# Optimization experiments

Measured on AMD Instinct MI355X. Metric: run time of the kernel, lower is better.

## Reference

```python
import jax, jax.numpy as jnp
import numpy as np

jax.config.update("jax_enable_x64", True)  # module does int64 wraparound hashing

# Derived from BloomFilter(num_items=10_000_000, false_positive_rate=0.01):
#   pre-round num_bits = ceil(1e7 * ln(100) / ln(2)^2) ~= 95,850,584
#   num_hashes = ceil(pre_round_bits / 1e7 * ln(2)) = 7
#   num_bits rounded up to power of two -> 2**27
NUM_BITS = 2 ** 27
BIT_MASK = NUM_BITS - 1
NUM_HASHES = 7
PRIME = 2654435761


def _hash(values):
    """(N,) int64 -> (N, k) bit positions. Matches torch: (v*PRIME + seed) & bit_mask
    (note Python precedence: & binds looser than +). int64 overflow wraps identically."""
    seeds = jnp.arange(NUM_HASHES, dtype=jnp.int64)
    return (values[:, None] * PRIME + seeds[None, :]) & BIT_MASK


def setup_inputs() -> dict:
    key = jax.random.key(0)
    k1, k2 = jax.random.split(key)
    add_values = jax.random.randint(k1, (4_000_000,), 0, 2**31 - 1, dtype=jnp.int64)
    query_values = jax.random.randint(k2, (8_000_000,), 0, 2**31 - 1, dtype=jnp.int64)
    return {"add_values": add_values, "query_values": query_values}


def reference(add_values, query_values):
    # Bit array of NUM_BITS bools. Semantically identical to the packed int64
    # bitset: word w, offset b in torch <-> flat index (w << 6) | b here, and a
    # bitwise-OR of single-bit masks is exactly an idempotent set-True scatter.
    bits = jnp.zeros((NUM_BITS,), dtype=bool)

    # add(): scatter-set all k hash positions of every inserted value
    add_pos = _hash(add_values)  # (M, k)
    bits = bits.at[add_pos.reshape(-1)].set(True)

    # contains(): gather k bits per query and AND-reduce
    q_pos = _hash(query_values)  # (N, k)
    return jnp.all(bits[q_pos], axis=1)  # (N,) bool
```

## Files before the change

kernel.cpp:

```cpp
#include <hip/hip_runtime.h>
#include <stdint.h>


#define NUM_BITS_LOG2 27
#define NUM_BITS (1u << NUM_BITS_LOG2)
#define BIT_MASK (NUM_BITS - 1u)
#define NUM_WORDS (NUM_BITS >> 6)
#define WORD_MASK (NUM_WORDS - 1u)
#define PRIME 2654435761u
#define H_WORDS (NUM_WORDS >> 2)

#define NBUCKETS 512
#define BKT_SHIFT (NUM_BITS_LOG2 - 9)
#define REGION_WORDS (1u << (BKT_SHIFT - 6))
#define H_WORDS_PER_REGION (REGION_WORDS / 4)
#define CAP 8688u
#define CHUNK 8192u
#define BLOCKS_A 512

typedef int vint4 __attribute__((ext_vector_type(4)));
typedef unsigned long long vull2 __attribute__((ext_vector_type(2)));

#define WS_H_ONLY 20971520ull
#define WS_FULL   38766592ull

__global__ __launch_bounds__(512) void init_gcnt_kernel(uint32_t* __restrict__ gcnt) {
    gcnt[threadIdx.x] = 0u;
}

__global__ __launch_bounds__(256) void scatter_kernel(
    const int* __restrict__ vals, int n,
    uint32_t* __restrict__ lists, uint32_t* __restrict__ gcnt)
{
    __shared__ uint32_t hist[NBUCKETS];
    __shared__ uint32_t sc[NBUCKETS];
    __shared__ uint32_t cur[NBUCKETS];
    __shared__ uint32_t gdelta[NBUCKETS];
    __shared__ uint32_t sortbuf[CHUNK];
    const uint32_t tid = threadIdx.x;
    const uint32_t un = (uint32_t)n;
    const uint32_t nchunks = (un + CHUNK - 1u) / CHUNK;

    for (uint32_t c = blockIdx.x; c < nchunks; c += gridDim.x) {
        const uint32_t base = c * CHUNK;
        const bool full = (base + CHUNK <= un);

        hist[tid] = 0u; hist[tid + 256] = 0u;
        __syncthreads();

        vint4 vv[8];
        if (full) {
            const vint4* src = (const vint4*)(vals + base);
            #pragma unroll
            for (int k = 0; k < 8; ++k) vv[k] = src[(uint32_t)k * 256u + tid];
            #pragma unroll
            for (int k = 0; k < 8; ++k) {
                #pragma unroll
                for (int j = 0; j < 4; ++j) {
                    uint32_t p = ((uint32_t)vv[k][j] * PRIME) & BIT_MASK;
                    uint32_t b1 = p >> BKT_SHIFT;
                    atomicAdd(&hist[b1], 1u);
                    uint32_t b2 = ((p + 6u) & BIT_MASK) >> BKT_SHIFT;
                    if (b2 != b1) {
                        uint32_t s2 = atomicAdd(&gcnt[b2], 1u);
                        if (s2 < CAP) lists[b2 * CAP + s2] = p;
                    }
                }
            }
        } else {
            #pragma unroll
            for (int k = 0; k < 32; ++k) {
                uint32_t idx = base + (uint32_t)k * 256u + tid;
                if (idx < un) {
                    uint32_t p = ((uint32_t)vals[idx] * PRIME) & BIT_MASK;
                    uint32_t b1 = p >> BKT_SHIFT;
                    atomicAdd(&hist[b1], 1u);
                    uint32_t b2 = ((p + 6u) & BIT_MASK) >> BKT_SHIFT;
                    if (b2 != b1) {
                        uint32_t s2 = atomicAdd(&gcnt[b2], 1u);
                        if (s2 < CAP) lists[b2 * CAP + s2] = p;
                    }
                }
            }
        }
        __syncthreads();

        sc[tid] = hist[tid]; sc[tid + 256] = hist[tid + 256];
        __syncthreads();
        for (uint32_t d = 1; d < NBUCKETS; d <<= 1) {
            uint32_t v0 = (tid >= d) ? sc[tid - d] : 0u;
            uint32_t v1 = (tid + 256u >= d) ? sc[tid + 256u - d] : 0u;
            __syncthreads();
            sc[tid] += v0; sc[tid + 256] += v1;
            __syncthreads();
        }

        #pragma unroll
        for (int q = 0; q < 2; ++q) {
            uint32_t i = tid + (uint32_t)q * 256u;
            uint32_t lb = i ? sc[i - 1] : 0u;
            uint32_t cc = hist[i];
            uint32_t go = cc ? atomicAdd(&gcnt[i], cc) : 0u;
            cur[i] = lb;
            gdelta[i] = i * CAP + go - lb;
        }
        __syncthreads();

        if (full) {
            #pragma unroll
            for (int k = 0; k < 8; ++k) {
                #pragma unroll
                for (int j = 0; j < 4; ++j) {
                    uint32_t p = ((uint32_t)vv[k][j] * PRIME) & BIT_MASK;
                    uint32_t b1 = p >> BKT_SHIFT;
                    uint32_t s = atomicAdd(&cur[b1], 1u);
                    sortbuf[s] = p;
                }
            }
        } else {
            #pragma unroll
            for (int k = 0; k < 32; ++k) {
                uint32_t idx = base + (uint32_t)k * 256u + tid;
                if (idx < un) {
                    uint32_t p = ((uint32_t)vals[idx] * PRIME) & BIT_MASK;
                    uint32_t b1 = p >> BKT_SHIFT;
                    uint32_t s = atomicAdd(&cur[b1], 1u);
                    sortbuf[s] = p;
                }
            }
        }
        __syncthreads();

        const uint32_t total = sc[NBUCKETS - 1];
        for (uint32_t i = tid; i < total; i += 256u) {
            uint32_t p = sortbuf[i];
            uint32_t b = p >> BKT_SHIFT;
            uint32_t dst = gdelta[b] + i;
            if (dst - b * CAP < CAP) lists[dst] = p;
        }
        __syncthreads();
    }
}

__device__ __forceinline__ void set_window(unsigned long long* bm, uint32_t p, uint32_t b) {
    int d = (int)((p - (b << BKT_SHIFT)) & BIT_MASK);
    if (d >= (1 << 26)) d -= (1 << 27);
    if (d < -6 || d >= (1 << BKT_SHIFT)) return;
    if (d < 0) {
        atomicOr(&bm[0], 0x7Full >> (uint32_t)(-d));
    } else {
        uint32_t w = (uint32_t)d >> 6, s = (uint32_t)d & 63u;
        atomicOr(&bm[w], 0x7Full << s);
        if (s > 57u) atomicOr(&bm[w + 1], 0x7Full >> (64u - s));
    }
}

__device__ __forceinline__ unsigned long long nib16(unsigned long long a) {
    unsigned long long t = a & (a >> 1);
    unsigned long long u = t & (t >> 2);
    u &= 0x1111111111111111ull;
    u |= u >> 3;  u &= 0x0303030303030303ull;
    u |= u >> 6;  u &= 0x000F000F000F000Full;
    u |= u >> 12; u &= 0x000000FF000000FFull;
    u |= u >> 24; return u & 0xFFFFull;
}

__global__ __launch_bounds__(256) void build_bitmap_kernel(
    const uint32_t* __restrict__ lists, const uint32_t* __restrict__ gcnt,
    unsigned long long* __restrict__ bits, unsigned long long* __restrict__ H)
{
    __shared__ unsigned long long bm[REGION_WORDS + 1];
    const uint32_t b = blockIdx.x, tid = threadIdx.x;
    for (uint32_t i = tid; i < REGION_WORDS + 1; i += 256) bm[i] = 0ull;
    __syncthreads();

    const uint32_t m = min(gcnt[b], CAP);
    const uint32_t base = b * CAP;
    for (uint32_t i = tid; i < m; i += 256) set_window(bm, lists[base + i], b);
    __syncthreads();

    const uint32_t out_base = b * REGION_WORDS;
    for (uint32_t i = tid; i < REGION_WORDS / 2; i += 256) {
        vull2 w; w[0] = bm[i * 2]; w[1] = bm[i * 2 + 1];
        *((vull2*)(bits + out_base) + i) = w;
    }
    const uint32_t h_base = b * H_WORDS_PER_REGION;
    for (uint32_t i = tid; i < H_WORDS_PER_REGION; i += 256) {
        unsigned long long hw = nib16(bm[i * 4])
                              | (nib16(bm[i * 4 + 1]) << 16)
                              | (nib16(bm[i * 4 + 2]) << 32)
                              | (nib16(bm[i * 4 + 3]) << 48);
        H[h_base + i] = hw;
    }
}

__device__ __forceinline__ int query_one_branchy(uint32_t v,
                                                 const unsigned long long* __restrict__ bits) {
    uint32_t p = (v * PRIME) & BIT_MASK;
    uint32_t w = p >> 6, s = p & 63u;
    unsigned long long lo = bits[w];
    unsigned long long win;
    if (s <= 57u) win = lo >> s;
    else win = (lo >> s) | (bits[(w + 1u) & WORD_MASK] << (64u - s));
    return ((win & 0x7Full) == 0x7Full) ? 1 : 0;
}

__global__ __launch_bounds__(256) void query_kernelH(
    const int* __restrict__ vals, int n,
    const unsigned long long* __restrict__ bits,
    const uint32_t* __restrict__ H32, int* __restrict__ out)
{
    int t = blockIdx.x * 256 + threadIdx.x;
    int base = t * 8;
    if (base + 7 < n) {
        vint4 v0 = __builtin_nontemporal_load((const vint4*)(vals + base));
        vint4 v1 = __builtin_nontemporal_load((const vint4*)(vals + base + 4));
        uint32_t p[8], pass[8];
        #pragma unroll
        for (int j = 0; j < 4; ++j) {
            p[j]     = ((uint32_t)v0[j] * PRIME) & BIT_MASK;
            p[j + 4] = ((uint32_t)v1[j] * PRIME) & BIT_MASK;
        }
        #pragma unroll
        for (int j = 0; j < 8; ++j) {
            uint32_t m = ((p[j] + 3u) & BIT_MASK) >> 2;
            pass[j] = (H32[m >> 5] >> (m & 31u)) & 1u;
        }
        unsigned long long lo[8], hi[8];
        uint32_t w[8], s[8];
        #pragma unroll
        for (int j = 0; j < 8; ++j) {
            w[j] = p[j] >> 6; s[j] = p[j] & 63u;
            lo[j] = 0ull; hi[j] = 0ull;
            if (pass[j]) lo[j] = bits[w[j]];
        }
        #pragma unroll
        for (int j = 0; j < 8; ++j) {
            if (pass[j] && s[j] > 57u)
                hi[j] = bits[(w[j] + 1u) & WORD_MASK];
        }
        vint4 r0, r1;
        #pragma unroll
        for (int j = 0; j < 8; ++j) {
            unsigned long long win = (lo[j] >> s[j]) | ((hi[j] << 1) << (63u - s[j]));
            int r = ((win & 0x7Full) == 0x7Full) ? 1 : 0;
            if (j < 4) r0[j] = r; else r1[j - 4] = r;
        }
        __builtin_nontemporal_store(r0, (vint4*)(out + base));
        __builtin_nontemporal_store(r1, (vint4*)(out + base + 4));
    } else {
        for (int j = base; j < n; ++j)
            out[j] = query_one_branchy((uint32_t)vals[j], bits);
    }
}

__global__ __launch_bounds__(256) void zero_bits_kernel(vull2* __restrict__ bits, int n2) {
    int i = blockIdx.x * 256 + threadIdx.x;
    if (i < n2) { vull2 z = {0ull, 0ull}; __builtin_nontemporal_store(z, &bits[i]); }
}

__device__ __forceinline__ void insert_one_atomic(uint32_t v,
                                                  unsigned long long* __restrict__ bits) {
    uint32_t p = (v * PRIME) & BIT_MASK;
    uint32_t w = p >> 6, s = p & 63u;
    atomicOr(bits + w, 0x7Full << s);
    if (s > 57u) atomicOr(bits + ((w + 1u) & WORD_MASK), 0x7Full >> (64u - s));
}

__global__ __launch_bounds__(256) void insert_atomic_kernel(const int* __restrict__ vals, int n,
                                                            unsigned long long* __restrict__ bits) {
    int t = blockIdx.x * 256 + threadIdx.x;
    int base = t * 4;
    if (base + 3 < n) {
        vint4 v = __builtin_nontemporal_load((const vint4*)vals + t);
        insert_one_atomic((uint32_t)v.x, bits);
        insert_one_atomic((uint32_t)v.y, bits);
        insert_one_atomic((uint32_t)v.z, bits);
        insert_one_atomic((uint32_t)v.w, bits);
    } else {
        for (int j = base; j < n; ++j) insert_one_atomic((uint32_t)vals[j], bits);
    }
}

__global__ __launch_bounds__(256) void build_h_kernel(
    const unsigned long long* __restrict__ bits, unsigned long long* __restrict__ H)
{
    uint32_t i = blockIdx.x * 256 + threadIdx.x;
    const vull2* b2 = (const vull2*)bits + (size_t)i * 2;
    vull2 a = b2[0];
    vull2 b = b2[1];
    unsigned long long hw = nib16(a[0])
                          | (nib16(a[1]) << 16)
                          | (nib16(b[0]) << 32)
                          | (nib16(b[1]) << 48);
    H[i] = hw;
}

__global__ __launch_bounds__(256) void query_kernel8(
    const int* __restrict__ vals, int n,
    const unsigned long long* __restrict__ bits, int* __restrict__ out)
{
    int t = blockIdx.x * 256 + threadIdx.x;
    int base = t * 8;
    if (base + 7 < n) {
        vint4 v0 = __builtin_nontemporal_load((const vint4*)(vals + base));
        vint4 v1 = __builtin_nontemporal_load((const vint4*)(vals + base + 4));
        vint4 r0, r1;
        #pragma unroll
        for (int j = 0; j < 8; ++j) {
            uint32_t v = (uint32_t)(j < 4 ? v0[j] : v1[j - 4]);
            int r = query_one_branchy(v, bits);
            if (j < 4) r0[j] = r; else r1[j - 4] = r;
        }
        __builtin_nontemporal_store(r0, (vint4*)(out + base));
        __builtin_nontemporal_store(r1, (vint4*)(out + base + 4));
    } else {
        for (int j = base; j < n; ++j)
            out[j] = query_one_branchy((uint32_t)vals[j], bits);
    }
}

extern "C" void kernel_launch(void* const* d_in, const int* in_sizes, int n_in,
                              void* d_out, int out_size, void* d_ws, size_t ws_size,
                              hipStream_t stream) {
    const int* add_values   = (const int*)d_in[0];
    const int* query_values = (const int*)d_in[1];
    const int n_add   = in_sizes[0];
    const int n_query = in_sizes[1];
    int* out = (int*)d_out;

    uint8_t* ws = (uint8_t*)d_ws;
    unsigned long long* bits = (unsigned long long*)ws;
    unsigned long long* H    = (unsigned long long*)(ws + 16777216);
    uint32_t* lists = (uint32_t*)(ws + 20971520);
    uint32_t* gcnt  = (uint32_t*)(ws + 38764544);

    const int threads = (n_query + 7) / 8;

    if (ws_size >= WS_FULL) {
        init_gcnt_kernel<<<1, 512, 0, stream>>>(gcnt);
        scatter_kernel<<<BLOCKS_A, 256, 0, stream>>>(add_values, n_add, lists, gcnt);
        build_bitmap_kernel<<<NBUCKETS, 256, 0, stream>>>(lists, gcnt, bits, H);
        query_kernelH<<<(threads + 255) / 256, 256, 0, stream>>>(
            query_values, n_query, bits, (const uint32_t*)H, out);
    } else if (ws_size >= WS_H_ONLY) {
        const int n2 = NUM_WORDS / 2;
        zero_bits_kernel<<<(n2 + 255) / 256, 256, 0, stream>>>((vull2*)bits, n2);
        const int threads4 = (n_add + 3) / 4;
        insert_atomic_kernel<<<(threads4 + 255) / 256, 256, 0, stream>>>(
            add_values, n_add, bits);
        build_h_kernel<<<H_WORDS / 256, 256, 0, stream>>>(bits, H);
        query_kernelH<<<(threads + 255) / 256, 256, 0, stream>>>(
            query_values, n_query, bits, (const uint32_t*)H, out);
    } else {
        const int n2 = NUM_WORDS / 2;
        zero_bits_kernel<<<(n2 + 255) / 256, 256, 0, stream>>>((vull2*)bits, n2);
        const int threads4 = (n_add + 3) / 4;
        insert_atomic_kernel<<<(threads4 + 255) / 256, 256, 0, stream>>>(
            add_values, n_add, bits);
        query_kernel8<<<(threads + 255) / 256, 256, 0, stream>>>(
            query_values, n_query, bits, out);
    }
}
```

Measured before the change: 186.4 us.

## Widen scatter/build blocks to 512 threads, use wave-shuffle scan, 16 queries per thread

The scatter kernel now runs 512 threads per block, one block per chunk, and replaces the shared-memory Hillis-Steele scan with a two-level wavefront shuffle scan, cutting barrier count. The bitmap build kernel also runs 512 threads per block. The query kernel handles 16 queries per thread with a pass bitmask and an occupancy hint, giving more memory-level parallelism for the gathers. In exchange it raises register pressure in the query kernel and changes the grid shapes.

After: 196.4 us. +5.4%, slower.

```diff
diff --git a/kernel.cpp b/kernel.cpp
--- a/kernel.cpp
+++ b/kernel.cpp
@@ -16,7 +16,6 @@
 #define H_WORDS_PER_REGION (REGION_WORDS / 4)
 #define CAP 8688u
 #define CHUNK 8192u
-#define BLOCKS_A 512
 
 typedef int vint4 __attribute__((ext_vector_type(4)));
 typedef unsigned long long vull2 __attribute__((ext_vector_type(2)));
@@ -28,16 +27,20 @@
     gcnt[threadIdx.x] = 0u;
 }
 
-__global__ __launch_bounds__(256) void scatter_kernel(
+__global__ __launch_bounds__(512) void scatter_kernel(
     const int* __restrict__ vals, int n,
     uint32_t* __restrict__ lists, uint32_t* __restrict__ gcnt)
 {
     __shared__ uint32_t hist[NBUCKETS];
-    __shared__ uint32_t sc[NBUCKETS];
     __shared__ uint32_t cur[NBUCKETS];
     __shared__ uint32_t gdelta[NBUCKETS];
+    __shared__ uint32_t wsum[8];
+    __shared__ uint32_t wexc[8];
+    __shared__ uint32_t total_s;
     __shared__ uint32_t sortbuf[CHUNK];
     const uint32_t tid = threadIdx.x;
+    const uint32_t lane = tid & 63u;
+    const uint32_t wv = tid >> 6;
     const uint32_t un = (uint32_t)n;
     const uint32_t nchunks = (un + CHUNK - 1u) / CHUNK;
 
@@ -45,16 +48,16 @@
         const uint32_t base = c * CHUNK;
         const bool full = (base + CHUNK <= un);
 
-        hist[tid] = 0u; hist[tid + 256] = 0u;
-        __syncthreads();
-
-        vint4 vv[8];
+        hist[tid] = 0u;
+        __syncthreads();
+
+        vint4 vv[4];
         if (full) {
             const vint4* src = (const vint4*)(vals + base);
             #pragma unroll
-            for (int k = 0; k < 8; ++k) vv[k] = src[(uint32_t)k * 256u + tid];
-            #pragma unroll
-            for (int k = 0; k < 8; ++k) {
+            for (int k = 0; k < 4; ++k) vv[k] = src[(uint32_t)k * 512u + tid];
+            #pragma unroll
+            for (int k = 0; k < 4; ++k) {
                 #pragma unroll
                 for (int j = 0; j < 4; ++j) {
                     uint32_t p = ((uint32_t)vv[k][j] * PRIME) & BIT_MASK;
@@ -69,8 +72,8 @@
             }
         } else {
             #pragma unroll
-            for (int k = 0; k < 32; ++k) {
-                uint32_t idx = base + (uint32_t)k * 256u + tid;
+            for (int k = 0; k < 16; ++k) {
+                uint32_t idx = base + (uint32_t)k * 512u + tid;
                 if (idx < un) {
                     uint32_t p = ((uint32_t)vals[idx] * PRIME) & BIT_MASK;
                     uint32_t b1 = p >> BKT_SHIFT;
@@ -85,30 +88,37 @@
         }
         __syncthreads();
 
-        sc[tid] = hist[tid]; sc[tid + 256] = hist[tid + 256];
-        __syncthreads();
-        for (uint32_t d = 1; d < NBUCKETS; d <<= 1) {
-            uint32_t v0 = (tid >= d) ? sc[tid - d] : 0u;
-            uint32_t v1 = (tid + 256u >= d) ? sc[tid + 256u - d] : 0u;
-            __syncthreads();
-            sc[tid] += v0; sc[tid + 256] += v1;
-            __syncthreads();
-        }
-
-        #pragma unroll
-        for (int q = 0; q < 2; ++q) {
-            uint32_t i = tid + (uint32_t)q * 256u;
-            uint32_t lb = i ? sc[i - 1] : 0u;
-            uint32_t cc = hist[i];
-            uint32_t go = cc ? atomicAdd(&gcnt[i], cc) : 0u;
-            cur[i] = lb;
-            gdelta[i] = i * CAP + go - lb;
-        }
+        const uint32_t c0 = hist[tid];
+        uint32_t x = c0;
+        #pragma unroll
+        for (uint32_t d = 1; d < 64; d <<= 1) {
+            uint32_t y = __shfl_up(x, d, 64);
+            if (lane >= d) x += y;
+        }
+        if (lane == 63u) wsum[wv] = x;
+        __syncthreads();
+        if (wv == 0) {
+            uint32_t t8 = (lane < 8u) ? wsum[lane] : 0u;
+            #pragma unroll
+            for (uint32_t d = 1; d < 8; d <<= 1) {
+                uint32_t y = __shfl_up(t8, d, 64);
+                if (lane >= d) t8 += y;
+            }
+            if (lane < 8u) wexc[lane] = t8 - wsum[lane];
+        }
+        __syncthreads();
+        const uint32_t inc = x + wexc[wv];
+        const uint32_t lb = inc - c0;
+        if (tid == NBUCKETS - 1) total_s = inc;
+
+        uint32_t go = c0 ? atomicAdd(&gcnt[tid], c0) : 0u;
+        cur[tid] = lb;
+        gdelta[tid] = tid * CAP + go - lb;
         __syncthreads();
 
         if (full) {
             #pragma unroll
-            for (int k = 0; k < 8; ++k) {
+            for (int k = 0; k < 4; ++k) {
                 #pragma unroll
                 for (int j = 0; j < 4; ++j) {
                     uint32_t p = ((uint32_t)vv[k][j] * PRIME) & BIT_MASK;
@@ -119,8 +129,8 @@
             }
         } else {
             #pragma unroll
-            for (int k = 0; k < 32; ++k) {
-                uint32_t idx = base + (uint32_t)k * 256u + tid;
+            for (int k = 0; k < 16; ++k) {
+                uint32_t idx = base + (uint32_t)k * 512u + tid;
                 if (idx < un) {
                     uint32_t p = ((uint32_t)vals[idx] * PRIME) & BIT_MASK;
                     uint32_t b1 = p >> BKT_SHIFT;
@@ -131,8 +141,8 @@
         }
         __syncthreads();
 
-        const uint32_t total = sc[NBUCKETS - 1];
-        for (uint32_t i = tid; i < total; i += 256u) {
+        const uint32_t total = total_s;
+        for (uint32_t i = tid; i < total; i += 512u) {
             uint32_t p = sortbuf[i];
             uint32_t b = p >> BKT_SHIFT;
             uint32_t dst = gdelta[b] + i;
@@ -165,27 +175,27 @@
     u |= u >> 24; return u & 0xFFFFull;
 }
 
-__global__ __launch_bounds__(256) void build_bitmap_kernel(
+__global__ __launch_bounds__(512) void build_bitmap_kernel(
     const uint32_t* __restrict__ lists, const uint32_t* __restrict__ gcnt,
     unsigned long long* __restrict__ bits, unsigned long long* __restrict__ H)
 {
     __shared__ unsigned long long bm[REGION_WORDS + 1];
     const uint32_t b = blockIdx.x, tid = threadIdx.x;
-    for (uint32_t i = tid; i < REGION_WORDS + 1; i += 256) bm[i] = 0ull;
+    for (uint32_t i = tid; i < REGION_WORDS + 1; i += 512) bm[i] = 0ull;
     __syncthreads();
 
     const uint32_t m = min(gcnt[b], CAP);
     const uint32_t base = b * CAP;
-    for (uint32_t i = tid; i < m; i += 256) set_window(bm, lists[base + i], b);
+    for (uint32_t i = tid; i < m; i += 512) set_window(bm, lists[base + i], b);
     __syncthreads();
 
     const uint32_t out_base = b * REGION_WORDS;
-    for (uint32_t i = tid; i < REGION_WORDS / 2; i += 256) {
+    for (uint32_t i = tid; i < REGION_WORDS / 2; i += 512) {
         vull2 w; w[0] = bm[i * 2]; w[1] = bm[i * 2 + 1];
         *((vull2*)(bits + out_base) + i) = w;
     }
     const uint32_t h_base = b * H_WORDS_PER_REGION;
-    for (uint32_t i = tid; i < H_WORDS_PER_REGION; i += 256) {
+    for (uint32_t i = tid; i < H_WORDS_PER_REGION; i += 512) {
         unsigned long long hw = nib16(bm[i * 4])
                               | (nib16(bm[i * 4 + 1]) << 16)
                               | (nib16(bm[i * 4 + 2]) << 32)
@@ -205,49 +215,53 @@
     return ((win & 0x7Full) == 0x7Full) ? 1 : 0;
 }
 
-__global__ __launch_bounds__(256) void query_kernelH(
+__global__ __launch_bounds__(256, 4) void query_kernelH(
     const int* __restrict__ vals, int n,
     const unsigned long long* __restrict__ bits,
     const uint32_t* __restrict__ H32, int* __restrict__ out)
 {
     int t = blockIdx.x * 256 + threadIdx.x;
-    int base = t * 8;
-    if (base + 7 < n) {
-        vint4 v0 = __builtin_nontemporal_load((const vint4*)(vals + base));
-        vint4 v1 = __builtin_nontemporal_load((const vint4*)(vals + base + 4));
-        uint32_t p[8], pass[8];
-        #pragma unroll
-        for (int j = 0; j < 4; ++j) {
-            p[j]     = ((uint32_t)v0[j] * PRIME) & BIT_MASK;
-            p[j + 4] = ((uint32_t)v1[j] * PRIME) & BIT_MASK;
-        }
-        #pragma unroll
-        for (int j = 0; j < 8; ++j) {
+    int base = t * 16;
+    if (base + 15 < n) {
+        vint4 v[4];
+        #pragma unroll
+        for (int k = 0; k < 4; ++k)
+            v[k] = __builtin_nontemporal_load((const vint4*)(vals + base) + k);
+        uint32_t p[16];
+        #pragma unroll
+        for (int k = 0; k < 4; ++k)
+            #pragma unroll
+            for (int j = 0; j < 4; ++j)
+                p[k * 4 + j] = ((uint32_t)v[k][j] * PRIME) & BIT_MASK;
+        uint32_t pb = 0u;
+        #pragma unroll
+        for (int j = 0; j < 16; ++j) {
             uint32_t m = ((p[j] + 3u) & BIT_MASK) >> 2;
-            pass[j] = (H32[m >> 5] >> (m & 31u)) & 1u;
-        }
-        unsigned long long lo[8], hi[8];
-        uint32_t w[8], s[8];
-        #pragma unroll
-        for (int j = 0; j < 8; ++j) {
-            w[j] = p[j] >> 6; s[j] = p[j] & 63u;
+            pb |= ((H32[m >> 5] >> (m & 31u)) & 1u) << j;
+        }
+        unsigned long long lo[16], hi[16];
+        #pragma unroll
+        for (int j = 0; j < 16; ++j) {
             lo[j] = 0ull; hi[j] = 0ull;
-            if (pass[j]) lo[j] = bits[w[j]];
-        }
-        #pragma unroll
-        for (int j = 0; j < 8; ++j) {
-            if (pass[j] && s[j] > 57u)
-                hi[j] = bits[(w[j] + 1u) & WORD_MASK];
-        }
-        vint4 r0, r1;
-        #pragma unroll
-        for (int j = 0; j < 8; ++j) {
-            unsigned long long win = (lo[j] >> s[j]) | ((hi[j] << 1) << (63u - s[j]));
-            int r = ((win & 0x7Full) == 0x7Full) ? 1 : 0;
-            if (j < 4) r0[j] = r; else r1[j - 4] = r;
-        }
-        __builtin_nontemporal_store(r0, (vint4*)(out + base));
-        __builtin_nontemporal_store(r1, (vint4*)(out + base + 4));
+            if ((pb >> j) & 1u) lo[j] = bits[p[j] >> 6];
+        }
+        #pragma unroll
+        for (int j = 0; j < 16; ++j) {
+            if (((pb >> j) & 1u) && (p[j] & 63u) > 57u)
+                hi[j] = bits[((p[j] >> 6) + 1u) & WORD_MASK];
+        }
+        #pragma unroll
+        for (int k = 0; k < 4; ++k) {
+            vint4 r;
+            #pragma unroll
+            for (int j = 0; j < 4; ++j) {
+                uint32_t s = p[k * 4 + j] & 63u;
+                unsigned long long win = (lo[k * 4 + j] >> s)
+                                       | ((hi[k * 4 + j] << 1) << (63u - s));
+                r[j] = ((win & 0x7Full) == 0x7Full) ? 1 : 0;
+            }
+            __builtin_nontemporal_store(r, (vint4*)(out + base) + k);
+        }
     } else {
         for (int j = base; j < n; ++j)
             out[j] = query_one_branchy((uint32_t)vals[j], bits);
@@ -335,13 +349,13 @@
     uint32_t* lists = (uint32_t*)(ws + 20971520);
     uint32_t* gcnt  = (uint32_t*)(ws + 38764544);
 
-    const int threads = (n_query + 7) / 8;
-
     if (ws_size >= WS_FULL) {
+        const uint32_t nchunks = ((uint32_t)n_add + CHUNK - 1u) / CHUNK;
         init_gcnt_kernel<<<1, 512, 0, stream>>>(gcnt);
-        scatter_kernel<<<BLOCKS_A, 256, 0, stream>>>(add_values, n_add, lists, gcnt);
-        build_bitmap_kernel<<<NBUCKETS, 256, 0, stream>>>(lists, gcnt, bits, H);
-        query_kernelH<<<(threads + 255) / 256, 256, 0, stream>>>(
+        scatter_kernel<<<nchunks, 512, 0, stream>>>(add_values, n_add, lists, gcnt);
+        build_bitmap_kernel<<<NBUCKETS, 512, 0, stream>>>(lists, gcnt, bits, H);
+        const int threads16 = (n_query + 15) / 16;
+        query_kernelH<<<(threads16 + 255) / 256, 256, 0, stream>>>(
             query_values, n_query, bits, (const uint32_t*)H, out);
     } else if (ws_size >= WS_H_ONLY) {
         const int n2 = NUM_WORDS / 2;
@@ -350,7 +364,8 @@
         insert_atomic_kernel<<<(threads4 + 255) / 256, 256, 0, stream>>>(
             add_values, n_add, bits);
         build_h_kernel<<<H_WORDS / 256, 256, 0, stream>>>(bits, H);
-        query_kernelH<<<(threads + 255) / 256, 256, 0, stream>>>(
+        const int threads16 = (n_query + 15) / 16;
+        query_kernelH<<<(threads16 + 255) / 256, 256, 0, stream>>>(
             query_values, n_query, bits, (const uint32_t*)H, out);
     } else {
         const int n2 = NUM_WORDS / 2;
@@ -358,7 +373,8 @@
         const int threads4 = (n_add + 3) / 4;
         insert_atomic_kernel<<<(threads4 + 255) / 256, 256, 0, stream>>>(
             add_values, n_add, bits);
-        query_kernel8<<<(threads + 255) / 256, 256, 0, stream>>>(
+        const int threads8 = (n_query + 7) / 8;
+        query_kernel8<<<(threads8 + 255) / 256, 256, 0, stream>>>(
             query_values, n_query, bits, out);
     }
 }
```
